# Kernel optimization log

Measured on AMD Instinct MI355X. Metric: run time of the kernel, lower is better.

The kernel has to match this reference:

```python
import jax, jax.numpy as jnp
import numpy as np

ALPHA = 0.01
BETA = 3e-05
OUT_H, OUT_W = 256, 256
KSIZE, SIGMA = 5, 4.0


def _gaussian_kernel2d(ks=KSIZE, sigma=SIGMA):
    x = jnp.arange(ks, dtype=jnp.float32) - (ks - 1) / 2.0
    g = jnp.exp(-(x * x) / (2.0 * sigma * sigma))
    g = g / g.sum()
    return jnp.outer(g, g)  # [ks, ks]


def _gaussian_blur(maps):
    # maps: [B, H, W]; reflect padding + depthwise 5x5 gaussian (kornia-style GaussianBlur2d)
    k = _gaussian_kernel2d()[None, None]  # [1,1,5,5]
    p = KSIZE // 2
    x = jnp.pad(maps[:, None], ((0, 0), (0, 0), (p, p), (p, p)), mode='reflect')
    y = jax.lax.conv_general_dilated(x, k, (1, 1), 'VALID')
    return y[:, 0]


def _resize_bilinear_align_corners(x, oh, ow):
    # x: [B, h, w] -> [B, oh, ow], torch F.interpolate(mode='bilinear', align_corners=True)
    B, h, w = x.shape
    ys = jnp.linspace(0.0, h - 1.0, oh)
    xs = jnp.linspace(0.0, w - 1.0, ow)
    y0 = jnp.floor(ys).astype(jnp.int32)
    x0 = jnp.floor(xs).astype(jnp.int32)
    y1 = jnp.minimum(y0 + 1, h - 1)
    x1 = jnp.minimum(x0 + 1, w - 1)
    fy = (ys - y0.astype(ys.dtype))[:, None]  # [oh,1]
    fx = (xs - x0.astype(xs.dtype))[None, :]  # [1,ow]
    a = x[:, y0][:, :, x0]
    b = x[:, y0][:, :, x1]
    c = x[:, y1][:, :, x0]
    d = x[:, y1][:, :, x1]
    top = a * (1.0 - fx) + b * fx
    bot = c * (1.0 - fx) + d * fx
    return top * (1.0 - fy) + bot * fy


def setup_inputs() -> dict:
    key = jax.random.key(0)
    k0, k1, k2 = jax.random.split(key, 3)
    B = 256
    return {
        'out0': jax.random.normal(k0, (B, 64, 64), jnp.float32),
        'out1': jax.random.normal(k1, (B, 32, 32), jnp.float32),
        'out2': jax.random.normal(k2, (B, 16, 16), jnp.float32),
    }


def reference(out0, out1, out2):
    outputs = [out0, out1, out2]
    B = out0.shape[0]
    # per-sample max of each scale -> softmax-weighted selection of per-sample weight
    max_vals = jnp.stack([o.reshape(B, -1).max(axis=1) for o in outputs], axis=1)  # [B,3]
    probs = jax.nn.softmax(max_vals, axis=1)
    mask = probs > probs.mean(axis=1, keepdims=True)  # probs > prob_mean
    cnt = mask.sum(axis=1)
    sel_mean = (max_vals * mask).sum(axis=1) / jnp.maximum(cnt, 1)
    total_weights = jnp.where(cnt > 0, jnp.maximum(sel_mean * ALPHA, BETA), BETA)  # [B]
    # multi-scale fusion: bilinear(align_corners=True) upsample to (256,256) and sum
    maps = _resize_bilinear_align_corners(out0, OUT_H, OUT_W)
    maps = maps + _resize_bilinear_align_corners(out1, OUT_H, OUT_W)
    maps = maps + _resize_bilinear_align_corners(out2, OUT_H, OUT_W)
    # gaussian blur then per-sample score. torch takes topk(k=f(total_weights)).values[0],
    # and topk values are sorted descending, so values[0] == max (k / total_weights drop out).
    blurred = _gaussian_blur(maps)
    scores = blurred.reshape(B, -1).max(axis=1)
    del total_weights  # only influenced the (unused) top-k size in the original
    return scores[:, None], maps
```

## Files before the change

kernel.cpp:

```cpp
#include <hip/hip_runtime.h>
#include <math.h>


static constexpr int W  = 256;
static constexpr int QB = 16;

__device__ __forceinline__ int reflect256(int i) {
    if (i < 0) i = -i;
    if (i > 255) i = 510 - i;
    return i;
}

__global__ __launch_bounds__(256, 4) void fused_kernel(
    const float* __restrict__ in0,
    const float* __restrict__ in1,
    const float* __restrict__ in2,
    float* __restrict__ part,
    float* __restrict__ maps)
{
    const int t   = threadIdx.x;
    const int q   = t & 63;
    const int wv  = __builtin_amdgcn_readfirstlane(t >> 6);
    const int bid = blockIdx.x;
    const int b   = bid >> 4;
    const int r0  = (bid & 15) * 16;
    const int rw0 = r0 + wv * 4;
    const int c0  = q * 4;

    const int rlo = max(r0 - 2, 0);
    const int rhi = min(r0 + 17, 255);
    const int y0lo = (rlo * 63) / 255;
    const int y1lo = (rlo * 31) / 255;
    const int y2lo = (rlo * 15) / 255;
    const int y0hi = min((rhi * 63) / 255 + 1, 63);
    const int y1hi = min((rhi * 31) / 255 + 1, 31);
    const int y2hi = min((rhi * 15) / 255 + 1, 15);
    const int n0 = y0hi - y0lo + 1;
    const int n1 = y1hi - y1lo + 1;
    const int n2 = y2hi - y2lo + 1;

    __shared__ float lds[4544];
    float* const s0r = lds;
    float* const s1r = lds + 448;
    float* const s2r = lds + 608;
    float* const xr0 = lds + 448;
    float* const xr1 = lds + 2240;
    float* const xr2 = lds + 3520;

    {
        const float4* g0 = (const float4*)(in0 + (size_t)b * 4096 + y0lo * 64);
        const float4* g1 = (const float4*)(in1 + (size_t)b * 1024 + y1lo * 32);
        const float4* g2 = (const float4*)(in2 + (size_t)b * 256  + y2lo * 16);
        if (t < n0 * 16) ((float4*)s0r)[t] = g0[t];
        if (t < n1 * 8)  ((float4*)s1r)[t] = g1[t];
        if (t < n2 * 4)  ((float4*)s2r)[t] = g2[t];
    }
    __syncthreads();

    const float inv255 = 1.0f / 255.0f;

    {
        int ix = t * 31; int xa = ix / 255; float fx = (float)(ix - 255 * xa) * inv255; int xb = min(xa + 1, 31);
        for (int r = 0; r < n1; ++r) {
            float a = s1r[r * 32 + xa], bv = s1r[r * 32 + xb];
            xr1[r * 256 + t] = a + fx * (bv - a);
        }
        ix = t * 15; xa = ix / 255; fx = (float)(ix - 255 * xa) * inv255; xb = min(xa + 1, 15);
        for (int r = 0; r < n2; ++r) {
            float a = s2r[r * 16 + xa], bv = s2r[r * 16 + xb];
            xr2[r * 256 + t] = a + fx * (bv - a);
        }
    }
    __syncthreads();

    {
        int ix = t * 63; int xa = ix / 255; float fx = (float)(ix - 255 * xa) * inv255; int xb = min(xa + 1, 63);
        for (int r = 0; r < n0; ++r) {
            float a = s0r[r * 64 + xa], bv = s0r[r * 64 + xb];
            xr0[r * 256 + t] = a + fx * (bv - a);
        }
    }
    __syncthreads();

    auto sample = [&](int rn, float* o) {
        const int ry = reflect256(rn);
        int iy = ry * 63; int ya = iy / 255; float w0 = (float)(iy - 255 * ya) * inv255; int ya1 = min(ya + 1, 63);
        int ib = ry * 31; int yb = ib / 255; float w1 = (float)(ib - 255 * yb) * inv255; int yb1 = min(yb + 1, 31);
        int ic = ry * 15; int yc = ic / 255; float w2 = (float)(ic - 255 * yc) * inv255; int yc1 = min(yc + 1, 15);
        const float4 l0 = *(const float4*)(xr0 + (ya  - y0lo) * 256 + c0);
        const float4 h0 = *(const float4*)(xr0 + (ya1 - y0lo) * 256 + c0);
        const float4 l1 = *(const float4*)(xr1 + (yb  - y1lo) * 256 + c0);
        const float4 h1 = *(const float4*)(xr1 + (yb1 - y1lo) * 256 + c0);
        const float4 l2 = *(const float4*)(xr2 + (yc  - y2lo) * 256 + c0);
        const float4 h2 = *(const float4*)(xr2 + (yc1 - y2lo) * 256 + c0);
        o[0] = (l0.x + w0 * (h0.x - l0.x)) + (l1.x + w1 * (h1.x - l1.x)) + (l2.x + w2 * (h2.x - l2.x));
        o[1] = (l0.y + w0 * (h0.y - l0.y)) + (l1.y + w1 * (h1.y - l1.y)) + (l2.y + w2 * (h2.y - l2.y));
        o[2] = (l0.z + w0 * (h0.z - l0.z)) + (l1.z + w1 * (h1.z - l1.z)) + (l2.z + w2 * (h2.z - l2.z));
        o[3] = (l0.w + w0 * (h0.w - l0.w)) + (l1.w + w1 * (h1.w - l1.w)) + (l2.w + w2 * (h2.w - l2.w));
    };

    const float e1 = expf(-1.0f / 32.0f);
    const float e2 = expf(-4.0f / 32.0f);
    const float nrm = 1.0f + 2.0f * e1 + 2.0f * e2;
    const float gwc = 1.0f / nrm, gwa = e1 / nrm, gwb = e2 / nrm;

    float m0[4], m1[4], m2[4], m3[4], mn[4];
    sample(rw0 - 2, m0);
    sample(rw0 - 1, m1);
    sample(rw0,     m2);
    sample(rw0 + 1, m3);

    float* __restrict__ mpr = maps + ((size_t)b * W + (size_t)rw0) * W + c0;
    *(float4*)(mpr)     = make_float4(m2[0], m2[1], m2[2], m2[3]);
    *(float4*)(mpr + W) = make_float4(m3[0], m3[1], m3[2], m3[3]);

    float gmax = -INFINITY;

#pragma unroll
    for (int i = 0; i < 4; ++i) {
        sample(rw0 + 2 + i, mn);

        if (i < 2)
            *(float4*)(mpr + (size_t)(2 + i) * W) = make_float4(mn[0], mn[1], mn[2], mn[3]);

        float vr0 = gwb * (m0[0] + mn[0]) + gwa * (m1[0] + m3[0]) + gwc * m2[0];
        float vr1 = gwb * (m0[1] + mn[1]) + gwa * (m1[1] + m3[1]) + gwc * m2[1];
        float vr2 = gwb * (m0[2] + mn[2]) + gwa * (m1[2] + m3[2]) + gwc * m2[2];
        float vr3 = gwb * (m0[3] + mn[3]) + gwa * (m1[3] + m3[3]) + gwc * m2[3];
#pragma unroll
        for (int k = 0; k < 4; ++k) { m0[k] = m1[k]; m1[k] = m2[k]; m2[k] = m3[k]; m3[k] = mn[k]; }

        float az = __shfl_up(vr2, 1);
        float aw = __shfl_up(vr3, 1);
        float cx = __shfl_down(vr0, 1);
        float cy = __shfl_down(vr1, 1);
        float a2 = (q == 0)  ? vr2 : az;
        float a3 = (q == 0)  ? vr1 : aw;
        float c4 = (q == 63) ? vr2 : cx;
        float c5 = (q == 63) ? vr1 : cy;
        float o0 = gwc * vr0 + gwa * (a3 + vr1)  + gwb * (a2 + vr2);
        float o1 = gwc * vr1 + gwa * (vr0 + vr2) + gwb * (a3 + vr3);
        float o2 = gwc * vr2 + gwa * (vr1 + vr3) + gwb * (vr0 + c4);
        float o3 = gwc * vr3 + gwa * (vr2 + c4)  + gwb * (vr1 + c5);
        gmax = fmaxf(gmax, fmaxf(fmaxf(o0, o1), fmaxf(o2, o3)));
    }

#pragma unroll
    for (int off = 32; off > 0; off >>= 1)
        gmax = fmaxf(gmax, __shfl_down(gmax, off));
    if (q == 0) part[bid * 4 + wv] = gmax;
}

__global__ void reduce_kernel(const float* __restrict__ part,
                              float* __restrict__ scores, int B) {
    int i = blockIdx.x * blockDim.x + threadIdx.x;
    if (i < B) {
        const float4* p = (const float4*)(part + 64 * i);
        float m = -INFINITY;
#pragma unroll
        for (int k = 0; k < 16; ++k) {
            float4 v = p[k];
            m = fmaxf(m, fmaxf(fmaxf(v.x, v.y), fmaxf(v.z, v.w)));
        }
        scores[i] = m;
    }
}

extern "C" void kernel_launch(void* const* d_in, const int* in_sizes, int n_in,
                              void* d_out, int out_size, void* d_ws, size_t ws_size,
                              hipStream_t stream) {
    const float* in0 = (const float*)d_in[0];
    const float* in1 = (const float*)d_in[1];
    const float* in2 = (const float*)d_in[2];
    const int B = in_sizes[0] / (64 * 64);

    float* scores = (float*)d_out;
    float* maps   = (float*)d_out + B;
    float* part   = (float*)d_ws;

    hipLaunchKernelGGL(fused_kernel, dim3(B * QB), dim3(256), 0, stream,
                       in0, in1, in2, part, maps);
    hipLaunchKernelGGL(reduce_kernel, dim3((B + 255) / 256), dim3(256), 0, stream,
                       part, scores, B);
}
```

Baseline: 92.13 us.

## Vectorize horizontal interpolation and step vertical interpolation incrementally across rows

Horizontal upsampling now has each thread produce four adjacent output columns from three shared source values and write them as a float4. All three scales run in one phase, which removes a barrier; the LDS layout is rebased so the source and intermediate rows no longer overlap. Vertical interpolation keeps the low and high rows in registers and advances a fractional remainder each output row, loading a new row only when the source index crosses. This avoids per-row integer divisions and six LDS loads per sample, at the cost of more registers and divergent boundary paths for reflect-padded rows.

```diff
diff --git a/kernel.cpp b/kernel.cpp
--- a/kernel.cpp
+++ b/kernel.cpp
@@ -39,13 +39,13 @@
     const int n1 = y1hi - y1lo + 1;
     const int n2 = y2hi - y2lo + 1;
 
-    __shared__ float lds[4544];
+    __shared__ float lds[4768];
     float* const s0r = lds;
     float* const s1r = lds + 448;
     float* const s2r = lds + 608;
-    float* const xr0 = lds + 448;
-    float* const xr1 = lds + 2240;
-    float* const xr2 = lds + 3520;
+    float* const xr0 = lds + 672;
+    float* const xr1 = lds + 2464;
+    float* const xr2 = lds + 3744;
 
     {
         const float4* g0 = (const float4*)(in0 + (size_t)b * 4096 + y0lo * 64);
@@ -60,43 +60,140 @@
     const float inv255 = 1.0f / 255.0f;
 
     {
-        int ix = t * 31; int xa = ix / 255; float fx = (float)(ix - 255 * xa) * inv255; int xb = min(xa + 1, 31);
-        for (int r = 0; r < n1; ++r) {
-            float a = s1r[r * 32 + xa], bv = s1r[r * 32 + xb];
-            xr1[r * 256 + t] = a + fx * (bv - a);
-        }
-        ix = t * 15; xa = ix / 255; fx = (float)(ix - 255 * xa) * inv255; xb = min(xa + 1, 15);
-        for (int r = 0; r < n2; ++r) {
-            float a = s2r[r * 16 + xa], bv = s2r[r * 16 + xb];
-            xr2[r * 256 + t] = a + fx * (bv - a);
+        const int T0 = n0 * 64;
+        for (int task = t; task < T0; task += 256) {
+            const int r = task >> 6, cq = (task & 63) * 4;
+            const float* src = s0r + r * 64;
+            const int x0 = (cq * 63) / 255;
+            const float v0 = src[x0];
+            const float v1 = src[min(x0 + 1, 63)];
+            const float v2 = src[min(x0 + 2, 63)];
+            float o[4];
+#pragma unroll
+            for (int k = 0; k < 4; ++k) {
+                const int ix = (cq + k) * 63;
+                const int xk = ix / 255;
+                const float fx = (float)(ix - 255 * xk) * inv255;
+                const float a  = (xk == x0) ? v0 : v1;
+                const float bb = (xk == x0) ? v1 : v2;
+                o[k] = a + fx * (bb - a);
+            }
+            *(float4*)(xr0 + r * 256 + cq) = make_float4(o[0], o[1], o[2], o[3]);
+        }
+        const int T1 = n1 * 64;
+        for (int task = t; task < T1; task += 256) {
+            const int r = task >> 6, cq = (task & 63) * 4;
+            const float* src = s1r + r * 32;
+            const int x0 = (cq * 31) / 255;
+            const float v0 = src[x0];
+            const float v1 = src[min(x0 + 1, 31)];
+            const float v2 = src[min(x0 + 2, 31)];
+            float o[4];
+#pragma unroll
+            for (int k = 0; k < 4; ++k) {
+                const int ix = (cq + k) * 31;
+                const int xk = ix / 255;
+                const float fx = (float)(ix - 255 * xk) * inv255;
+                const float a  = (xk == x0) ? v0 : v1;
+                const float bb = (xk == x0) ? v1 : v2;
+                o[k] = a + fx * (bb - a);
+            }
+            *(float4*)(xr1 + r * 256 + cq) = make_float4(o[0], o[1], o[2], o[3]);
+        }
+        const int T2 = n2 * 64;
+        for (int task = t; task < T2; task += 256) {
+            const int r = task >> 6, cq = (task & 63) * 4;
+            const float* src = s2r + r * 16;
+            const int x0 = (cq * 15) / 255;
+            const float v0 = src[x0];
+            const float v1 = src[min(x0 + 1, 15)];
+            const float v2 = src[min(x0 + 2, 15)];
+            float o[4];
+#pragma unroll
+            for (int k = 0; k < 4; ++k) {
+                const int ix = (cq + k) * 15;
+                const int xk = ix / 255;
+                const float fx = (float)(ix - 255 * xk) * inv255;
+                const float a  = (xk == x0) ? v0 : v1;
+                const float bb = (xk == x0) ? v1 : v2;
+                o[k] = a + fx * (bb - a);
+            }
+            *(float4*)(xr2 + r * 256 + cq) = make_float4(o[0], o[1], o[2], o[3]);
         }
     }
     __syncthreads();
 
-    {
-        int ix = t * 63; int xa = ix / 255; float fx = (float)(ix - 255 * xa) * inv255; int xb = min(xa + 1, 63);
-        for (int r = 0; r < n0; ++r) {
-            float a = s0r[r * 64 + xa], bv = s0r[r * 64 + xb];
-            xr0[r * 256 + t] = a + fx * (bv - a);
-        }
-    }
-    __syncthreads();
-
-    auto sample = [&](int rn, float* o) {
+    auto ld0 = [&](int y, float* d) {
+        const float4 v = *(const float4*)(xr0 + (y - y0lo) * 256 + c0);
+        d[0] = v.x; d[1] = v.y; d[2] = v.z; d[3] = v.w;
+    };
+    auto ld1 = [&](int y, float* d) {
+        const float4 v = *(const float4*)(xr1 + (y - y1lo) * 256 + c0);
+        d[0] = v.x; d[1] = v.y; d[2] = v.z; d[3] = v.w;
+    };
+    auto ld2 = [&](int y, float* d) {
+        const float4 v = *(const float4*)(xr2 + (y - y2lo) * 256 + c0);
+        d[0] = v.x; d[1] = v.y; d[2] = v.z; d[3] = v.w;
+    };
+
+    int ya, yb, yc, rem0, rem1, rem2;
+    float rl0[4], rh0[4], rl1[4], rh1[4], rl2[4], rh2[4];
+
+    auto init_state = [&](int rn) {
+        int iy;
+        iy = rn * 63; ya = iy / 255; rem0 = iy - 255 * ya; ld0(ya, rl0); ld0(min(ya + 1, 63), rh0);
+        iy = rn * 31; yb = iy / 255; rem1 = iy - 255 * yb; ld1(yb, rl1); ld1(min(yb + 1, 31), rh1);
+        iy = rn * 15; yc = iy / 255; rem2 = iy - 255 * yc; ld2(yc, rl2); ld2(min(yc + 1, 15), rh2);
+    };
+
+    auto step = [&](float* o) {
+        const float w0 = (float)rem0 * inv255;
+        const float w1 = (float)rem1 * inv255;
+        const float w2 = (float)rem2 * inv255;
+#pragma unroll
+        for (int k = 0; k < 4; ++k) {
+            o[k] = (rl0[k] + w0 * (rh0[k] - rl0[k]))
+                 + (rl1[k] + w1 * (rh1[k] - rl1[k]))
+                 + (rl2[k] + w2 * (rh2[k] - rl2[k]));
+        }
+        rem0 += 63;
+        if (rem0 >= 255) {
+            rem0 -= 255; ++ya;
+#pragma unroll
+            for (int k = 0; k < 4; ++k) rl0[k] = rh0[k];
+            ld0(min(ya + 1, 63), rh0);
+        }
+        rem1 += 31;
+        if (rem1 >= 255) {
+            rem1 -= 255; ++yb;
+#pragma unroll
+            for (int k = 0; k < 4; ++k) rl1[k] = rh1[k];
+            ld1(min(yb + 1, 31), rh1);
+        }
+        rem2 += 15;
+        if (rem2 >= 255) {
+            rem2 -= 255; ++yc;
+#pragma unroll
+            for (int k = 0; k < 4; ++k) rl2[k] = rh2[k];
+            ld2(min(yc + 1, 15), rh2);
+        }
+    };
+
+    auto direct4 = [&](int rn, float* o) {
         const int ry = reflect256(rn);
-        int iy = ry * 63; int ya = iy / 255; float w0 = (float)(iy - 255 * ya) * inv255; int ya1 = min(ya + 1, 63);
-        int ib = ry * 31; int yb = ib / 255; float w1 = (float)(ib - 255 * yb) * inv255; int yb1 = min(yb + 1, 31);
-        int ic = ry * 15; int yc = ic / 255; float w2 = (float)(ic - 255 * yc) * inv255; int yc1 = min(yc + 1, 15);
-        const float4 l0 = *(const float4*)(xr0 + (ya  - y0lo) * 256 + c0);
-        const float4 h0 = *(const float4*)(xr0 + (ya1 - y0lo) * 256 + c0);
-        const float4 l1 = *(const float4*)(xr1 + (yb  - y1lo) * 256 + c0);
-        const float4 h1 = *(const float4*)(xr1 + (yb1 - y1lo) * 256 + c0);
-        const float4 l2 = *(const float4*)(xr2 + (yc  - y2lo) * 256 + c0);
-        const float4 h2 = *(const float4*)(xr2 + (yc1 - y2lo) * 256 + c0);
-        o[0] = (l0.x + w0 * (h0.x - l0.x)) + (l1.x + w1 * (h1.x - l1.x)) + (l2.x + w2 * (h2.x - l2.x));
-        o[1] = (l0.y + w0 * (h0.y - l0.y)) + (l1.y + w1 * (h1.y - l1.y)) + (l2.y + w2 * (h2.y - l2.y));
-        o[2] = (l0.z + w0 * (h0.z - l0.z)) + (l1.z + w1 * (h1.z - l1.z)) + (l2.z + w2 * (h2.z - l2.z));
-        o[3] = (l0.w + w0 * (h0.w - l0.w)) + (l1.w + w1 * (h1.w - l1.w)) + (l2.w + w2 * (h2.w - l2.w));
+        int iy = ry * 63; int a0 = iy / 255; float w0 = (float)(iy - 255 * a0) * inv255; int a1 = min(a0 + 1, 63);
+        int ib = ry * 31; int b0 = ib / 255; float w1 = (float)(ib - 255 * b0) * inv255; int b1 = min(b0 + 1, 31);
+        int ic = ry * 15; int cc0 = ic / 255; float w2 = (float)(ic - 255 * cc0) * inv255; int cc1 = min(cc0 + 1, 15);
+        float l0[4], h0[4], l1[4], h1[4], l2[4], h2[4];
+        ld0(a0, l0); ld0(a1, h0);
+        ld1(b0, l1); ld1(b1, h1);
+        ld2(cc0, l2); ld2(cc1, h2);
+#pragma unroll
+        for (int k = 0; k < 4; ++k) {
+            o[k] = (l0[k] + w0 * (h0[k] - l0[k]))
+                 + (l1[k] + w1 * (h1[k] - l1[k]))
+                 + (l2[k] + w2 * (h2[k] - l2[k]));
+        }
     };
 
     const float e1 = expf(-1.0f / 32.0f);
@@ -105,10 +202,17 @@
     const float gwc = 1.0f / nrm, gwa = e1 / nrm, gwb = e2 / nrm;
 
     float m0[4], m1[4], m2[4], m3[4], mn[4];
-    sample(rw0 - 2, m0);
-    sample(rw0 - 1, m1);
-    sample(rw0,     m2);
-    sample(rw0 + 1, m3);
+    if (rw0 == 0) {
+        direct4(2, m0);
+        direct4(1, m1);
+        direct4(0, m2);
+#pragma unroll
+        for (int k = 0; k < 4; ++k) m3[k] = m1[k];
+        init_state(2);
+    } else {
+        init_state(rw0 - 2);
+        step(m0); step(m1); step(m2); step(m3);
+    }
 
     float* __restrict__ mpr = maps + ((size_t)b * W + (size_t)rw0) * W + c0;
     *(float4*)(mpr)     = make_float4(m2[0], m2[1], m2[2], m2[3]);
@@ -118,7 +222,9 @@
 
 #pragma unroll
     for (int i = 0; i < 4; ++i) {
-        sample(rw0 + 2 + i, mn);
+        const int rn = rw0 + 2 + i;
+        if (rn <= 255) step(mn);
+        else           direct4(rn, mn);
 
         if (i < 2)
             *(float4*)(mpr + (size_t)(2 + i) * W) = make_float4(mn[0], mn[1], mn[2], mn[3]);
```

Measured after the change: 99.68 us. 1.08x slower.
